# Kernel optimization log

Measured on AMD Instinct MI355X. Metric: run time of the kernel, lower is better.

Reference implementation:

```python
import jax, jax.numpy as jnp
import numpy as np

N = 100000      # nodes
E = 1600000     # edges
FX = 128        # raw node feature dim
MAXZ = 100      # z embedding / one-hot size
HID = 128       # hidden_channels
NL = 3          # num_layers
G = 512         # num graphs
BN_EPS = 1e-5


def _lin(key, din, dout):
    return jax.random.normal(key, (din, dout), jnp.float32) * (1.0 / np.sqrt(din))


def setup_inputs() -> dict:
    key = jax.random.key(0)
    ks = jax.random.split(key, 64)
    d = {}
    d["x"] = jax.random.normal(ks[0], (N, FX), jnp.float32)
    d["z"] = jax.random.randint(ks[1], (N,), 0, MAXZ)
    d["edge_index"] = jax.random.randint(ks[2], (2, E), 0, N)
    d["batch"] = jnp.sort(jax.random.randint(ks[3], (N,), 0, G))
    in0 = FX + 2 * MAXZ  # z_emb concatenated twice (faithful to source)
    ki = 4
    for l in range(NL):
        din = in0 if l == 0 else HID
        d[f"W1_{l}"] = _lin(ks[ki], din, HID); ki += 1
        d[f"b1_{l}"] = jnp.zeros((HID,), jnp.float32)
        d[f"W2_{l}"] = _lin(ks[ki], HID, HID); ki += 1
        d[f"b2_{l}"] = jnp.zeros((HID,), jnp.float32)
        d[f"g_{l}"] = jnp.ones((HID,), jnp.float32)
        d[f"be_{l}"] = jnp.zeros((HID,), jnp.float32)
    d["Wl1"] = _lin(ks[ki], NL * HID, HID); ki += 1
    d["bl1"] = jnp.zeros((HID,), jnp.float32)
    d["Wl2"] = _lin(ks[ki], HID, 1); ki += 1
    d["bl2"] = jnp.zeros((1,), jnp.float32)
    return d


def _gin_layer(h, src, dst, W1, b1, W2, b2, g, be):
    # GINConv with eps=0: nn(x + sum_{j->i} x_j)
    agg = jax.ops.segment_sum(h[src], dst, num_segments=N)  # [N, d]
    m = h + agg
    m = jax.nn.relu(m @ W1 + b1)
    m = jax.nn.relu(m @ W2 + b2)
    # training-mode BatchNorm1d over node axis (biased variance)
    mu = m.mean(0)
    var = jnp.mean((m - mu) ** 2, axis=0)
    return (m - mu) * jax.lax.rsqrt(var + BN_EPS) * g + be


def reference(x, z, edge_index, batch,
              W1_0, b1_0, W2_0, b2_0, g_0, be_0,
              W1_1, b1_1, W2_1, b2_1, g_1, be_1,
              W1_2, b1_2, W2_2, b2_2, g_2, be_2,
              Wl1, bl1, Wl2, bl2):
    src, dst = edge_index[0], edge_index[1]
    z_emb = jax.nn.one_hot(z, MAXZ, dtype=jnp.float32)  # [N, MAXZ]
    h = jnp.concatenate([z_emb, x], axis=1)
    h = jnp.concatenate([z_emb, h], axis=1)  # faithful double concat -> [N, FX+2*MAXZ]
    params = [(W1_0, b1_0, W2_0, b2_0, g_0, be_0),
              (W1_1, b1_1, W2_1, b2_1, g_1, be_1),
              (W1_2, b1_2, W2_2, b2_2, g_2, be_2)]
    xs = []
    for p in params:
        h = _gin_layer(h, src, dst, *p)
        xs.append(h)
    hcat = jnp.concatenate(xs, axis=1)  # jumping knowledge: [N, NL*HID]
    # global_mean_pool over graph ids
    counts = jax.ops.segment_sum(jnp.ones((N,), jnp.float32), batch, num_segments=G)
    pooled = jax.ops.segment_sum(hcat, batch, num_segments=G) / jnp.maximum(counts, 1.0)[:, None]
    out = jax.nn.relu(pooled @ Wl1 + bl1)
    # dropout is identity in eval / reference mode
    out = out @ Wl2 + bl2  # [G, 1]
    return out
```

## Files before the change

kernel.cpp:

```cpp
#include <hip/hip_runtime.h>
#include <hip/hip_bf16.h>

#define NN 100000
#define NROWS_PAD 100032
#define EE 1600000
#define GG 512
#define NPB 256
#define NB  ((NN + NPB - 1) / NPB)
#define PCHUNK 4096
#define PBLOCKS ((EE + PCHUNK - 1) / PCHUNK)
#define SBANK 8
static constexpr float BN_EPS = 1e-5f;

typedef _Float16 half8 __attribute__((ext_vector_type(8)));
typedef float floatx4 __attribute__((ext_vector_type(4)));


__global__ __launch_bounds__(256) void k_bhist(const int* __restrict__ EI,
                                               int* __restrict__ bcount)
{
    __shared__ int h[NB];
    const int t = threadIdx.x;
    for (int i = t; i < NB; i += 256) h[i] = 0;
    __syncthreads();
    const int e0 = blockIdx.x * PCHUNK;
    const int e1 = (e0 + PCHUNK < EE) ? e0 + PCHUNK : EE;
    for (int e = e0 + t; e < e1; e += 256)
        atomicAdd(&h[EI[EE + e] >> 8], 1);
    __syncthreads();
    for (int i = t; i < NB; i += 256)
        if (h[i]) atomicAdd(&bcount[i], h[i]);
}

__global__ __launch_bounds__(512) void k_bscan(const int* __restrict__ bcount,
                                               int* __restrict__ bstart,
                                               int* __restrict__ bcursor,
                                               int* __restrict__ row_start)
{
    __shared__ int s[512];
    int t = threadIdx.x;
    int v = (t < NB) ? bcount[t] : 0;
    s[t] = v;
    __syncthreads();
    for (int off = 1; off < 512; off <<= 1) {
        int u = (t >= off) ? s[t - off] : 0;
        __syncthreads();
        s[t] += u;
        __syncthreads();
    }
    if (t < NB) { int ex = s[t] - v; bstart[t] = ex; bcursor[t] = ex; }
    if (t == 0) { bstart[NB] = EE; row_start[NN] = EE; }
}

__global__ __launch_bounds__(256) void k_part(const int* __restrict__ EI,
                                              int* __restrict__ bcursor,
                                              int* __restrict__ ebuf)
{
    __shared__ int h[NB];
    __shared__ int cur[NB];
    const int t = threadIdx.x;
    for (int i = t; i < NB; i += 256) h[i] = 0;
    __syncthreads();
    const int e0 = blockIdx.x * PCHUNK;
    const int e1 = (e0 + PCHUNK < EE) ? e0 + PCHUNK : EE;
    for (int e = e0 + t; e < e1; e += 256)
        atomicAdd(&h[EI[EE + e] >> 8], 1);
    __syncthreads();
    for (int i = t; i < NB; i += 256)
        cur[i] = h[i] ? atomicAdd(&bcursor[i], h[i]) : 0;
    __syncthreads();
    for (int e = e0 + t; e < e1; e += 256) {
        int s = EI[e], d = EI[EE + e];
        int pos = atomicAdd(&cur[d >> 8], 1);
        ebuf[pos] = s | ((d & (NPB - 1)) << 17);
    }
}

__global__ __launch_bounds__(256) void k_csrbucket(const int* __restrict__ ebuf,
                                                   const int* __restrict__ bstart,
                                                   int* __restrict__ row_start,
                                                   int* __restrict__ ssrc)
{
    __shared__ int cnt[NPB];
    __shared__ int cur[NPB];
    const int b = blockIdx.x, t = threadIdx.x;
    cnt[t] = 0;
    __syncthreads();
    const int e0 = bstart[b], e1 = bstart[b + 1];
    for (int e = e0 + t; e < e1; e += 256) {
        unsigned p = (unsigned)__builtin_nontemporal_load(&ebuf[e]);
        atomicAdd(&cnt[p >> 17], 1);
    }
    __syncthreads();
    int myc = cnt[t];
    for (int off = 1; off < 256; off <<= 1) {
        int u = (t >= off) ? cnt[t - off] : 0;
        __syncthreads();
        cnt[t] += u;
        __syncthreads();
    }
    int pos0 = e0 + cnt[t] - myc;
    int idx = b * NPB + t;
    if (idx < NN) row_start[idx] = pos0;
    cur[t] = pos0;
    __syncthreads();
    for (int e = e0 + t; e < e1; e += 256) {
        unsigned p = (unsigned)__builtin_nontemporal_load(&ebuf[e]);
        int pos = atomicAdd(&cur[p >> 17], 1);
        ssrc[pos] = (int)(p & 0x1FFFFu);
    }
}


__global__ __launch_bounds__(128) void k_bnfold(
    const float* __restrict__ statsL,
    const float* __restrict__ g, const float* __restrict__ be,
    float* __restrict__ scsh)
{
    int k = threadIdx.x;
    float cs = 0.f, cq = 0.f;
    #pragma unroll
    for (int b = 0; b < SBANK; ++b) {
        cs += statsL[b * 256 + k];
        cq += statsL[b * 256 + 128 + k];
    }
    float inv_n = 1.0f / (float)NN;
    float mu = cs * inv_n;
    float var = cq * inv_n - mu * mu;
    float sc = g[k] * rsqrtf(var + BN_EPS);
    scsh[k] = sc;
    scsh[128 + k] = be[k] - mu * sc;
}

__global__ __launch_bounds__(256) void k_prep(
    const float* __restrict__ W1, const float* __restrict__ W2,
    const float* __restrict__ scsh,
    _Float16* __restrict__ Wt1, _Float16* __restrict__ Wt2,
    float* __restrict__ cvec, int l)
{
    __shared__ float shs[128];
    int b = blockIdx.x, t = threadIdx.x;
    if (b < 64) {
        int idx = b * 256 + t;
        int n = idx >> 7, k = idx & 127;
        if (l == 0)
            Wt1[idx] = (_Float16)W1[(200 + k) * 128 + n];
        else
            Wt1[idx] = (_Float16)(scsh[k] * W1[k * 128 + n]);
    } else if (b < 128) {
        int idx = (b - 64) * 256 + t;
        int n = idx >> 7, k = idx & 127;
        Wt2[idx] = (_Float16)W2[k * 128 + n];
    } else {
        if (t < 128) shs[t] = (l != 0) ? scsh[128 + t] : 0.f;
        __syncthreads();
        if (t < 128) {
            float acc = 0.f;
            if (l != 0) {
                #pragma unroll 4
                for (int k = 0; k < 128; ++k)
                    acc = fmaf(shs[k], W1[k * 128 + t], acc);
            }
            cvec[t] = acc;
        }
    }
}


#define MM_CORE_G(Ah, Wth)                                                   \
    const int lane = tid & 63;                                               \
    const int wv = tid >> 6;                                                 \
    const int ml = lane & 15;                                                \
    const int quad = lane >> 4;                                              \
    const int wr = wv >> 1, wc = wv & 1;                                     \
    floatx4 acc[2][4];                                                       \
    for (int r = 0; r < 2; ++r)                                              \
        for (int t = 0; t < 4; ++t)                                          \
            acc[r][t] = (floatx4){0.f, 0.f, 0.f, 0.f};                       \
    {                                                                        \
        const size_t ar0 = (size_t)(row0 + 32 * wr + ml) * 128;              \
        const size_t ar1 = ar0 + (size_t)16 * 128;                           \
        _Pragma("unroll")                                                    \
        for (int kq = 0; kq < 4; ++kq) {                                     \
            int k0 = kq * 32;                                                \
            half8 a0 = *(const half8*)&Ah[ar0 + k0 + quad * 8];              \
            half8 a1 = *(const half8*)&Ah[ar1 + k0 + quad * 8];              \
            _Pragma("unroll")                                                \
            for (int t = 0; t < 4; ++t) {                                    \
                half8 bf = *(const half8*)&Wth[(size_t)(64 * wc + 16 * t + ml) * 128 + k0 + quad * 8]; \
                acc[0][t] = __builtin_amdgcn_mfma_f32_16x16x32_f16(a0, bf, acc[0][t], 0, 0, 0); \
                acc[1][t] = __builtin_amdgcn_mfma_f32_16x16x32_f16(a1, bf, acc[1][t], 0, 0, 0); \
            }                                                                \
        }                                                                    \
    }

#define MM_STORE_LDS(Csh, Out)                                               \
    __syncthreads();                                                         \
    _Pragma("unroll")                                                        \
    for (int c = 0; c < 4; ++c) {                                            \
        int chunk = tid * 8 + c * 2048;                                      \
        if (row0 + (chunk >> 7) < NN)                                        \
            *(half8*)&Out[(size_t)row0 * 128 + chunk] = *(const half8*)&Csh[chunk]; \
    }

__global__ __launch_bounds__(256) void k_mm_embed(
    const float* __restrict__ X, const _Float16* __restrict__ Wth,
    const int* __restrict__ Z, const float* __restrict__ W1,
    _Float16* __restrict__ Ph)
{
    __shared__ _Float16 Csh[64 * 128];
    const int tid = threadIdx.x;
    const int row0 = blockIdx.x * 64;
    const int lane = tid & 63;
    const int wv = tid >> 6;
    const int ml = lane & 15;
    const int quad = lane >> 4;
    const int wr = wv >> 1, wc = wv & 1;
    floatx4 acc[2][4];
    #pragma unroll
    for (int r = 0; r < 2; ++r)
        #pragma unroll
        for (int t = 0; t < 4; ++t)
            acc[r][t] = (floatx4){0.f, 0.f, 0.f, 0.f};
    int r0g = row0 + 32 * wr + ml;
    int r1g = r0g + 16;
    if (r0g > NN - 1) r0g = NN - 1;
    if (r1g > NN - 1) r1g = NN - 1;
    const float* x0 = &X[(size_t)r0g * 128];
    const float* x1 = &X[(size_t)r1g * 128];
    #pragma unroll
    for (int kq = 0; kq < 4; ++kq) {
        int k0 = kq * 32 + quad * 8;
        float4 f0a = *(const float4*)&x0[k0];
        float4 f0b = *(const float4*)&x0[k0 + 4];
        float4 f1a = *(const float4*)&x1[k0];
        float4 f1b = *(const float4*)&x1[k0 + 4];
        half8 a0 = { (_Float16)f0a.x, (_Float16)f0a.y, (_Float16)f0a.z, (_Float16)f0a.w,
                     (_Float16)f0b.x, (_Float16)f0b.y, (_Float16)f0b.z, (_Float16)f0b.w };
        half8 a1 = { (_Float16)f1a.x, (_Float16)f1a.y, (_Float16)f1a.z, (_Float16)f1a.w,
                     (_Float16)f1b.x, (_Float16)f1b.y, (_Float16)f1b.z, (_Float16)f1b.w };
        #pragma unroll
        for (int t = 0; t < 4; ++t) {
            half8 bf = *(const half8*)&Wth[(size_t)(64 * wc + 16 * t + ml) * 128 + kq * 32 + quad * 8];
            acc[0][t] = __builtin_amdgcn_mfma_f32_16x16x32_f16(a0, bf, acc[0][t], 0, 0, 0);
            acc[1][t] = __builtin_amdgcn_mfma_f32_16x16x32_f16(a1, bf, acc[1][t], 0, 0, 0);
        }
    }
    #pragma unroll
    for (int r = 0; r < 2; ++r)
        #pragma unroll
        for (int j = 0; j < 4; ++j) {
            int lrow = 32 * wr + 16 * r + quad * 4 + j;
            int grow = row0 + lrow;
            int zv = (grow < NN) ? Z[grow] : 0;
            const float* w0 = &W1[zv * 128];
            const float* w1 = &W1[(100 + zv) * 128];
            #pragma unroll
            for (int t = 0; t < 4; ++t) {
                int gcol = 64 * wc + 16 * t + ml;
                Csh[lrow * 128 + gcol] = (_Float16)(acc[r][t][j] + w0[gcol] + w1[gcol]);
            }
        }
    MM_STORE_LDS(Csh, Ph)
}

__global__ __launch_bounds__(256) void k_mm1(
    const _Float16* __restrict__ Ah, const _Float16* __restrict__ Wth,
    _Float16* __restrict__ Ph)
{
    __shared__ _Float16 Csh[64 * 128];
    const int tid = threadIdx.x;
    const int row0 = blockIdx.x * 64;
    MM_CORE_G(Ah, Wth)
    #pragma unroll
    for (int r = 0; r < 2; ++r)
        #pragma unroll
        for (int j = 0; j < 4; ++j) {
            int lrow = 32 * wr + 16 * r + quad * 4 + j;
            #pragma unroll
            for (int t = 0; t < 4; ++t)
                Csh[lrow * 128 + 64 * wc + 16 * t + ml] = (_Float16)acc[r][t][j];
        }
    MM_STORE_LDS(Csh, Ph)
}

__global__ __launch_bounds__(256) void k_mm2(
    const _Float16* __restrict__ Ah, const _Float16* __restrict__ Wth,
    const float* __restrict__ b2, _Float16* __restrict__ Oh,
    float* __restrict__ statsL)
{
    __shared__ _Float16 Csh[64 * 128];
    __shared__ float cs[128];
    __shared__ float cq[128];
    const int tid = threadIdx.x;
    const int row0 = blockIdx.x * 64;
    if (tid < 128) { cs[tid] = 0.f; cq[tid] = 0.f; }
    __syncthreads();

    MM_CORE_G(Ah, Wth)

    float b2v[4];
    #pragma unroll
    for (int t = 0; t < 4; ++t) b2v[t] = b2[64 * wc + 16 * t + ml];
    float st[4] = {0.f, 0.f, 0.f, 0.f};
    float qt[4] = {0.f, 0.f, 0.f, 0.f};
    #pragma unroll
    for (int r = 0; r < 2; ++r)
        #pragma unroll
        for (int j = 0; j < 4; ++j) {
            int lrow = 32 * wr + 16 * r + quad * 4 + j;
            bool ok = (row0 + lrow) < NN;
            #pragma unroll
            for (int t = 0; t < 4; ++t) {
                int gcol = 64 * wc + 16 * t + ml;
                float v = ok ? fmaxf(acc[r][t][j] + b2v[t], 0.f) : 0.f;
                Csh[lrow * 128 + gcol] = (_Float16)v;
                st[t] += v;
                qt[t] += v * v;
            }
        }
    #pragma unroll
    for (int t = 0; t < 4; ++t) {
        int gcol = 64 * wc + 16 * t + ml;
        atomicAdd(&cs[gcol], st[t]);
        atomicAdd(&cq[gcol], qt[t]);
    }
    MM_STORE_LDS(Csh, Oh)
    if (tid < 128) {
        float* bank = statsL + (blockIdx.x & (SBANK - 1)) * 256;
        atomicAdd(&bank[tid], cs[tid]);
        atomicAdd(&bank[128 + tid], cq[tid]);
    }
}


__global__ __launch_bounds__(256) void k_aggregate(
    const _Float16* __restrict__ Ph, const int* __restrict__ row_start,
    const int* __restrict__ ssrc, const float* __restrict__ b1,
    const float* __restrict__ cvec, _Float16* __restrict__ Mh)
{
    int idx = blockIdx.x * 256 + threadIdx.x;
    int node = idx >> 4, q = idx & 15;
    if (node >= NN) return;
    int s0 = row_start[node], s1 = row_start[node + 1];
    float degp1 = (float)(s1 - s0 + 1);
    float acc[8];
    half8 pv = *(const half8*)&Ph[(size_t)node * 128 + q * 8];
    #pragma unroll
    for (int j = 0; j < 8; ++j)
        acc[j] = (float)pv[j] + fmaf(degp1, cvec[q * 8 + j], b1[q * 8 + j]);
    int e = s0;
    for (; e + 7 < s1; e += 8) {
        int sidx[8];
        #pragma unroll
        for (int u = 0; u < 8; ++u)
            sidx[u] = __builtin_nontemporal_load(&ssrc[e + u]);
        half8 v[8];
        #pragma unroll
        for (int u = 0; u < 8; ++u)
            v[u] = *(const half8*)&Ph[(size_t)sidx[u] * 128 + q * 8];
        #pragma unroll
        for (int j = 0; j < 8; ++j)
            acc[j] += (((float)v[0][j] + (float)v[1][j]) + ((float)v[2][j] + (float)v[3][j]))
                    + (((float)v[4][j] + (float)v[5][j]) + ((float)v[6][j] + (float)v[7][j]));
    }
    for (; e + 1 < s1; e += 2) {
        int sa = __builtin_nontemporal_load(&ssrc[e]);
        int sb = __builtin_nontemporal_load(&ssrc[e + 1]);
        half8 va = *(const half8*)&Ph[(size_t)sa * 128 + q * 8];
        half8 vb = *(const half8*)&Ph[(size_t)sb * 128 + q * 8];
        #pragma unroll
        for (int j = 0; j < 8; ++j) acc[j] += (float)va[j] + (float)vb[j];
    }
    if (e < s1) {
        int sa = __builtin_nontemporal_load(&ssrc[e]);
        half8 va = *(const half8*)&Ph[(size_t)sa * 128 + q * 8];
        #pragma unroll
        for (int j = 0; j < 8; ++j) acc[j] += (float)va[j];
    }
    half8 o;
    #pragma unroll
    for (int j = 0; j < 8; ++j) o[j] = (_Float16)fmaxf(acc[j], 0.f);
    __builtin_nontemporal_store(o, (half8*)&Mh[(size_t)node * 128 + q * 8]);
}


__global__ __launch_bounds__(256) void k_pool(
    const _Float16* __restrict__ Ah, const int* __restrict__ batch,
    const float* __restrict__ scsh,
    float* __restrict__ pooled, int loff)
{
    __shared__ float red[16][128];
    int g = blockIdx.x;
    int t = threadIdx.x;
    int rg = t >> 4, seg = t & 15;
    int lo = 0, hi = NN;
    while (lo < hi) { int mid = (lo + hi) >> 1; if (batch[mid] < g) lo = mid + 1; else hi = mid; }
    int s = lo;
    lo = s; hi = NN;
    while (lo < hi) { int mid = (lo + hi) >> 1; if (batch[mid] < g + 1) lo = mid + 1; else hi = mid; }
    int e = lo;
    float acc[8] = {};
    for (int i = s + rg; i < e; i += 16) {
        half8 v = *(const half8*)&Ah[(size_t)i * 128 + seg * 8];
        #pragma unroll
        for (int j = 0; j < 8; ++j) acc[j] += (float)v[j];
    }
    #pragma unroll
    for (int j = 0; j < 8; ++j) red[rg][seg * 8 + j] = acc[j];
    __syncthreads();
    int cnt = e - s;
    float inv = 1.0f / (float)(cnt > 0 ? cnt : 1);
    if (t < 128) {
        float s_ = 0.f;
        #pragma unroll
        for (int r = 0; r < 16; ++r) s_ += red[r][t];
        pooled[g * 384 + loff + t] = fmaf(scsh[t], s_ * inv, scsh[128 + t]);
    }
}

__global__ __launch_bounds__(128) void k_final(
    const float* __restrict__ pooled,
    const float* __restrict__ Wl1, const float* __restrict__ bl1,
    const float* __restrict__ Wl2, const float* __restrict__ bl2,
    float* __restrict__ out)
{
    __shared__ float pr[384];
    __shared__ float red[128];
    int g = blockIdx.x, j = threadIdx.x;
    for (int i = j; i < 384; i += 128) pr[i] = pooled[g * 384 + i];
    __syncthreads();
    float acc = bl1[j];
    for (int k = 0; k < 384; ++k) acc = fmaf(pr[k], Wl1[k * 128 + j], acc);
    float r = fmaxf(acc, 0.f) * Wl2[j];
    red[j] = r;
    __syncthreads();
    for (int off = 64; off > 0; off >>= 1) {
        if (j < off) red[j] += red[j + off];
        __syncthreads();
    }
    if (j == 0) out[g] = red[0] + bl2[0];
}

extern "C" void kernel_launch(void* const* d_in, const int* in_sizes, int n_in,
                              void* d_out, int out_size, void* d_ws, size_t ws_size,
                              hipStream_t stream)
{
    const float* x     = (const float*)d_in[0];
    const int*   z     = (const int*)d_in[1];
    const int*   ei    = (const int*)d_in[2];
    const int*   batch = (const int*)d_in[3];
    const float* W1a[3] = {(const float*)d_in[4],  (const float*)d_in[10], (const float*)d_in[16]};
    const float* b1a[3] = {(const float*)d_in[5],  (const float*)d_in[11], (const float*)d_in[17]};
    const float* W2a[3] = {(const float*)d_in[6],  (const float*)d_in[12], (const float*)d_in[18]};
    const float* b2a[3] = {(const float*)d_in[7],  (const float*)d_in[13], (const float*)d_in[19]};
    const float* ga[3]  = {(const float*)d_in[8],  (const float*)d_in[14], (const float*)d_in[20]};
    const float* bea[3] = {(const float*)d_in[9],  (const float*)d_in[15], (const float*)d_in[21]};
    const float* Wl1 = (const float*)d_in[22];
    const float* bl1 = (const float*)d_in[23];
    const float* Wl2 = (const float*)d_in[24];
    const float* bl2 = (const float*)d_in[25];
    float* out = (float*)d_out;

    char* ws = (char*)d_ws;
    size_t off = 0;
    auto alloc = [&](size_t bytes) {
        void* p = ws + off;
        off += (bytes + 255) & ~(size_t)255;
        return p;
    };
    _Float16* Ph  = (_Float16*)alloc((size_t)NROWS_PAD * 128 * 2);
    _Float16* Mh  = (_Float16*)alloc((size_t)NROWS_PAD * 128 * 2);
    _Float16* Ahb = (_Float16*)alloc((size_t)NROWS_PAD * 128 * 2);
    _Float16* Wt1 = (_Float16*)alloc((size_t)128 * 128 * 2);
    _Float16* Wt2 = (_Float16*)alloc((size_t)128 * 128 * 2);
    int*   ebuf     = (int*)alloc((size_t)EE * 4);
    int*   ssrc     = (int*)alloc((size_t)EE * 4);
    int*   row_st   = (int*)alloc((size_t)(NN + 1) * 4);
    int*   bcount   = (int*)alloc((size_t)NB * 4);
    int*   bstart   = (int*)alloc((size_t)(NB + 1) * 4);
    int*   bcursor  = (int*)alloc((size_t)NB * 4);
    float* cvec     = (float*)alloc(128 * 4);
    float* stats    = (float*)alloc((size_t)3 * SBANK * 256 * 4);
    float* scshA    = (float*)alloc((size_t)3 * 256 * 4);
    float* pooled   = (float*)alloc((size_t)GG * 384 * 4);

    const int gemmBlocks = (NN + 63) / 64;
    const int aggBlocks  = (NN * 16 + 255) / 256;

    hipMemsetAsync(stats, 0, (size_t)3 * SBANK * 256 * 4, stream);
    hipMemsetAsync(bcount, 0, (size_t)NB * 4, stream);
    k_bhist<<<PBLOCKS, 256, 0, stream>>>(ei, bcount);
    k_bscan<<<1, 512, 0, stream>>>(bcount, bstart, bcursor, row_st);
    k_part<<<PBLOCKS, 256, 0, stream>>>(ei, bcursor, ebuf);
    k_csrbucket<<<NB, 256, 0, stream>>>(ebuf, bstart, row_st, ssrc);

    const float* scshPrev = scshA;
    for (int l = 0; l < 3; ++l) {
        float* statsL = stats + (size_t)l * SBANK * 256;
        float* scshL  = scshA + (size_t)l * 256;
        k_prep<<<129, 256, 0, stream>>>(W1a[l], W2a[l], scshPrev, Wt1, Wt2, cvec, l);
        if (l == 0)
            k_mm_embed<<<gemmBlocks, 256, 0, stream>>>(x, Wt1, z, W1a[0], Ph);
        else
            k_mm1<<<gemmBlocks, 256, 0, stream>>>(Ahb, Wt1, Ph);
        k_aggregate<<<aggBlocks, 256, 0, stream>>>(Ph, row_st, ssrc, b1a[l], cvec, Mh);
        k_mm2<<<gemmBlocks, 256, 0, stream>>>(Mh, Wt2, b2a[l], Ahb, statsL);
        k_bnfold<<<1, 128, 0, stream>>>(statsL, ga[l], bea[l], scshL);
        k_pool<<<GG, 256, 0, stream>>>(Ahb, batch, scshL, pooled, l * 128);
        scshPrev = scshL;
    }
    k_final<<<GG, 128, 0, stream>>>(pooled, Wl1, bl1, Wl2, bl2, out);
}
```

Measured before the change: 634.9 us.

## Fuse graph mean-pooling into mm2 epilogue and defer BN affine to final

Removes the per-layer k_pool kernel. Each mm2 block now accumulates per-graph column sums of its pre-BN output tile straight from LDS into a raw pooled buffer using global atomics. A separate one-block kernel computes inverse graph counts, and k_final applies the mean and the BN scale/shift, which is valid because BN is affine. Also doubles the edge partition chunk size; atomics add contention and the pooled sum now uses fp16-rounded values.

```diff
diff --git a/kernel.cpp b/kernel.cpp
--- a/kernel.cpp
+++ b/kernel.cpp
@@ -7,7 +7,7 @@
 #define GG 512
 #define NPB 256
 #define NB  ((NN + NPB - 1) / NPB)
-#define PCHUNK 4096
+#define PCHUNK 8192
 #define PBLOCKS ((EE + PCHUNK - 1) / PCHUNK)
 #define SBANK 8
 static constexpr float BN_EPS = 1e-5f;
@@ -109,6 +109,20 @@
         int pos = atomicAdd(&cur[p >> 17], 1);
         ssrc[pos] = (int)(p & 0x1FFFFu);
     }
+}
+
+
+__global__ __launch_bounds__(512) void k_gcnt(const int* __restrict__ batch,
+                                              float* __restrict__ ginv)
+{
+    int g = threadIdx.x;
+    int lo = 0, hi = NN;
+    while (lo < hi) { int m = (lo + hi) >> 1; if (batch[m] < g) lo = m + 1; else hi = m; }
+    int s = lo;
+    lo = s; hi = NN;
+    while (lo < hi) { int m = (lo + hi) >> 1; if (batch[m] < g + 1) lo = m + 1; else hi = m; }
+    int c = lo - s;
+    ginv[g] = 1.0f / (float)(c > 0 ? c : 1);
 }
 
 
@@ -286,15 +300,18 @@
 
 __global__ __launch_bounds__(256) void k_mm2(
     const _Float16* __restrict__ Ah, const _Float16* __restrict__ Wth,
-    const float* __restrict__ b2, _Float16* __restrict__ Oh,
-    float* __restrict__ statsL)
+    const float* __restrict__ b2, const int* __restrict__ batch,
+    _Float16* __restrict__ Oh, float* __restrict__ statsL,
+    float* __restrict__ praw, int loff)
 {
     __shared__ _Float16 Csh[64 * 128];
     __shared__ float cs[128];
     __shared__ float cq[128];
+    __shared__ int bsh[64];
     const int tid = threadIdx.x;
     const int row0 = blockIdx.x * 64;
     if (tid < 128) { cs[tid] = 0.f; cq[tid] = 0.f; }
+    if (tid < 64) bsh[tid] = (row0 + tid < NN) ? batch[row0 + tid] : -1;
     __syncthreads();
 
     MM_CORE_G(Ah, Wth)
@@ -326,6 +343,22 @@
         atomicAdd(&cq[gcol], qt[t]);
     }
     MM_STORE_LDS(Csh, Oh)
+
+    {
+        int col = tid & 127;
+        int rbase = (tid >> 7) << 5;
+        float run = 0.f;
+        int curg = bsh[rbase];
+        for (int r = rbase; r < rbase + 32; ++r) {
+            int gg = bsh[r];
+            if (gg != curg) {
+                if (curg >= 0) atomicAdd(&praw[curg * 384 + loff + col], run);
+                run = 0.f; curg = gg;
+            }
+            run += (float)Csh[r * 128 + col];
+        }
+        if (curg >= 0) atomicAdd(&praw[curg * 384 + loff + col], run);
+    }
     if (tid < 128) {
         float* bank = statsL + (blockIdx.x & (SBANK - 1)) * 256;
         atomicAdd(&bank[tid], cs[tid]);
@@ -385,42 +418,9 @@
 }
 
 
-__global__ __launch_bounds__(256) void k_pool(
-    const _Float16* __restrict__ Ah, const int* __restrict__ batch,
-    const float* __restrict__ scsh,
-    float* __restrict__ pooled, int loff)
-{
-    __shared__ float red[16][128];
-    int g = blockIdx.x;
-    int t = threadIdx.x;
-    int rg = t >> 4, seg = t & 15;
-    int lo = 0, hi = NN;
-    while (lo < hi) { int mid = (lo + hi) >> 1; if (batch[mid] < g) lo = mid + 1; else hi = mid; }
-    int s = lo;
-    lo = s; hi = NN;
-    while (lo < hi) { int mid = (lo + hi) >> 1; if (batch[mid] < g + 1) lo = mid + 1; else hi = mid; }
-    int e = lo;
-    float acc[8] = {};
-    for (int i = s + rg; i < e; i += 16) {
-        half8 v = *(const half8*)&Ah[(size_t)i * 128 + seg * 8];
-        #pragma unroll
-        for (int j = 0; j < 8; ++j) acc[j] += (float)v[j];
-    }
-    #pragma unroll
-    for (int j = 0; j < 8; ++j) red[rg][seg * 8 + j] = acc[j];
-    __syncthreads();
-    int cnt = e - s;
-    float inv = 1.0f / (float)(cnt > 0 ? cnt : 1);
-    if (t < 128) {
-        float s_ = 0.f;
-        #pragma unroll
-        for (int r = 0; r < 16; ++r) s_ += red[r][t];
-        pooled[g * 384 + loff + t] = fmaf(scsh[t], s_ * inv, scsh[128 + t]);
-    }
-}
-
 __global__ __launch_bounds__(128) void k_final(
-    const float* __restrict__ pooled,
+    const float* __restrict__ praw, const float* __restrict__ ginv,
+    const float* __restrict__ scshA,
     const float* __restrict__ Wl1, const float* __restrict__ bl1,
     const float* __restrict__ Wl2, const float* __restrict__ bl2,
     float* __restrict__ out)
@@ -428,7 +428,12 @@
     __shared__ float pr[384];
     __shared__ float red[128];
     int g = blockIdx.x, j = threadIdx.x;
-    for (int i = j; i < 384; i += 128) pr[i] = pooled[g * 384 + i];
+    float gi = ginv[g];
+    for (int i = j; i < 384; i += 128) {
+        int l = i >> 7, c = i & 127;
+        pr[i] = fmaf(scshA[l * 256 + c], praw[g * 384 + i] * gi,
+                     scshA[l * 256 + 128 + c]);
+    }
     __syncthreads();
     float acc = bl1[j];
     for (int k = 0; k < 384; ++k) acc = fmaf(pr[k], Wl1[k * 128 + j], acc);
@@ -483,17 +488,20 @@
     float* cvec     = (float*)alloc(128 * 4);
     float* stats    = (float*)alloc((size_t)3 * SBANK * 256 * 4);
     float* scshA    = (float*)alloc((size_t)3 * 256 * 4);
-    float* pooled   = (float*)alloc((size_t)GG * 384 * 4);
+    float* praw     = (float*)alloc((size_t)GG * 384 * 4);
+    float* ginv     = (float*)alloc((size_t)GG * 4);
 
     const int gemmBlocks = (NN + 63) / 64;
     const int aggBlocks  = (NN * 16 + 255) / 256;
 
     hipMemsetAsync(stats, 0, (size_t)3 * SBANK * 256 * 4, stream);
     hipMemsetAsync(bcount, 0, (size_t)NB * 4, stream);
+    hipMemsetAsync(praw, 0, (size_t)GG * 384 * 4, stream);
     k_bhist<<<PBLOCKS, 256, 0, stream>>>(ei, bcount);
     k_bscan<<<1, 512, 0, stream>>>(bcount, bstart, bcursor, row_st);
     k_part<<<PBLOCKS, 256, 0, stream>>>(ei, bcursor, ebuf);
     k_csrbucket<<<NB, 256, 0, stream>>>(ebuf, bstart, row_st, ssrc);
+    k_gcnt<<<1, 512, 0, stream>>>(batch, ginv);
 
     const float* scshPrev = scshA;
     for (int l = 0; l < 3; ++l) {
@@ -505,10 +513,10 @@
         else
             k_mm1<<<gemmBlocks, 256, 0, stream>>>(Ahb, Wt1, Ph);
         k_aggregate<<<aggBlocks, 256, 0, stream>>>(Ph, row_st, ssrc, b1a[l], cvec, Mh);
-        k_mm2<<<gemmBlocks, 256, 0, stream>>>(Mh, Wt2, b2a[l], Ahb, statsL);
+        k_mm2<<<gemmBlocks, 256, 0, stream>>>(Mh, Wt2, b2a[l], batch, Ahb, statsL,
+                                              praw, l * 128);
         k_bnfold<<<1, 128, 0, stream>>>(statsL, ga[l], bea[l], scshL);
-        k_pool<<<GG, 256, 0, stream>>>(Ahb, batch, scshL, pooled, l * 128);
         scshPrev = scshL;
     }
-    k_final<<<GG, 128, 0, stream>>>(pooled, Wl1, bl1, Wl2, bl2, out);
-}
+    k_final<<<GG, 128, 0, stream>>>(praw, ginv, scshA, Wl1, bl1, Wl2, bl2, out);
+}
```

Measured after the change: 648.0 us. +2.1%, slower.
